# Kernel optimization log

Hardware: AMD Instinct MI355X
Metric: run time of the kernel (lower is better)

Reference implementation:

```python
import jax, jax.numpy as jnp
import numpy as np

B, C, H, W = 4, 512, 128, 128
CI = C // 2   # inter_planes
CQ = C // 8   # q/k dim in CrossAttention


def conv1x1(x, w, b=None):
    # x: [B,Cin,H,W], w: [Cout,Cin]
    y = jnp.einsum('oc,bchw->bohw', w, x)
    if b is not None:
        y = y + b[None, :, None, None]
    return y


def setup_inputs() -> dict:
    key = jax.random.key(0)
    ks = jax.random.split(key, 13)
    s = 0.05
    return {
        'x': jax.random.normal(ks[0], (B, C, H, W), jnp.float32),
        # SCCA gating params (1x1 convs, no bias except conv_up)
        'w_q_right': jax.random.normal(ks[1], (1, C), jnp.float32) * s,
        'w_v_right': jax.random.normal(ks[2], (CI, C), jnp.float32) * s,
        'w_up': jax.random.normal(ks[3], (C, CI), jnp.float32) * s,
        'b_up': jnp.zeros((C,), jnp.float32),
        'w_q_left': jax.random.normal(ks[4], (CI, C), jnp.float32) * s,
        'w_v_left': jax.random.normal(ks[5], (CI, C), jnp.float32) * s,
        # CrossAttention params (1x1 convs with bias)
        'wq': jax.random.normal(ks[6], (CQ, C), jnp.float32) * s,
        'bq': jnp.zeros((CQ,), jnp.float32),
        'wk': jax.random.normal(ks[7], (CQ, C), jnp.float32) * s,
        'bk': jnp.zeros((CQ,), jnp.float32),
        'wv': jax.random.normal(ks[8], (C, C), jnp.float32) * s,
        'bv': jnp.zeros((C,), jnp.float32),
        'gamma': jnp.asarray(0.5, jnp.float32),
    }


def cross_attention(x, wq, bq, wk, bk, wv, bv, gamma):
    # criss-cross attention: each pixel attends to its row and column
    b, c, h, w = x.shape
    q = conv1x1(x, wq, bq)   # [B,CQ,H,W]
    k = conv1x1(x, wk, bk)   # [B,CQ,H,W]
    v = conv1x1(x, wv, bv)   # [B,C,H,W]
    # column (H) affinities with -inf on the self diagonal (as in INF())
    diag = jnp.where(jnp.eye(h, dtype=bool), -jnp.inf, 0.0).astype(x.dtype)
    e_h = jnp.einsum('bchw,bcgw->bhwg', q, k) + diag[None, :, None, :]  # [B,H,W,H]
    e_w = jnp.einsum('bchw,bchv->bhwv', q, k)                            # [B,H,W,W]
    att = jax.nn.softmax(jnp.concatenate([e_h, e_w], axis=-1), axis=-1)  # [B,H,W,H+W]
    a_h, a_w = att[..., :h], att[..., h:]
    out_h = jnp.einsum('bcgw,bhwg->bchw', v, a_h)
    out_w = jnp.einsum('bchv,bhwv->bchw', v, a_w)
    return gamma * (out_h + out_w) + x


def spatial_weighted(x, w_q_right, w_v_right, w_up, b_up):
    b, c, h, w = x.shape
    input_x = conv1x1(x, w_v_right).reshape(b, CI, h * w)       # [B,CI,HW]
    mask = jax.nn.softmax(conv1x1(x, w_q_right).reshape(b, h * w), axis=-1)  # [B,HW]
    ctx = jnp.einsum('bcn,bn->bc', input_x, mask)               # [B,CI]
    ctx = jnp.einsum('oc,bc->bo', w_up, ctx) + b_up             # [B,C]
    mask_ch = jax.nn.sigmoid(ctx)[:, :, None, None]
    return x * mask_ch


def channel_weighted(x, w_q_left, w_v_left):
    b, c, h, w = x.shape
    g_x = conv1x1(x, w_q_left)                                  # [B,CI,H,W]
    avg = g_x.mean(axis=(2, 3))                                 # [B,CI]
    theta = conv1x1(x, w_v_left).reshape(b, CI, h * w)          # [B,CI,HW]
    ctx = jax.nn.softmax(jnp.einsum('bc,bcn->bn', avg, theta), axis=-1)
    mask_sp = jax.nn.sigmoid(ctx).reshape(b, 1, h, w)
    return x * mask_sp


def reference(x, w_q_right, w_v_right, w_up, b_up, w_q_left, w_v_left,
              wq, bq, wk, bk, wv, bv, gamma):
    cc = spatial_weighted(x, w_q_right, w_v_right, w_up, b_up)
    cc = cross_attention(cc, wq, bq, wk, bk, wv, bv, gamma)
    cs = channel_weighted(x, w_q_left, w_v_left)
    cs = cross_attention(cs, wq, bq, wk, bk, wv, bv, gamma)
    out = cs + cc
    out = cross_attention(out, wq, bq, wk, bk, wv, bv, gamma)
    return out
```

## Files before the change

### kernel.cpp

```cpp
#include <hip/hip_runtime.h>
#include <hip/hip_bf16.h>
#include <math.h>

typedef __hip_bfloat16 bf16;
typedef __attribute__((ext_vector_type(8))) short s16x8;
typedef __attribute__((ext_vector_type(4))) float f32x4;

constexpr int Bn  = 4;
constexpr int Cn  = 512;
constexpr int Hn  = 128;
constexpr int Wn  = 128;
constexpr int Nn  = Hn * Wn;
constexpr int CQn = 64;
constexpr int CIn = 256;

__device__ __forceinline__ float bf2f(bf16 v){ return __bfloat162float(v); }
__device__ __forceinline__ bf16  f2bf(float v){ return __float2bfloat16(v); }

__device__ __forceinline__ void gload_lds16(const void* g, void* l){
  __builtin_amdgcn_global_load_lds(
      (const __attribute__((address_space(1))) unsigned int*)g,
      (__attribute__((address_space(3))) unsigned int*)l,
      16, 0, 0);
}


__global__ __launch_bounds__(256) void k_dotc(const float* __restrict__ x,
                                              const float* __restrict__ w,
                                              int wstride,
                                              float* __restrict__ out){
  int t = blockIdx.x * 256 + threadIdx.x;
  int b = t >> 14;
  const float* wp = w + (size_t)b * wstride;
  const float* xp = x + (size_t)b * Cn * Nn + (t & (Nn - 1));
  float acc = 0.f;
  #pragma unroll 8
  for (int c = 0; c < Cn; ++c) acc += wp[c] * xp[(size_t)c * Nn];
  out[t] = acc;
}

__global__ __launch_bounds__(256) void k_rowmean(const float* __restrict__ x,
                                                 float* __restrict__ out,
                                                 float scale){
  int bc = blockIdx.x;
  const float* xp = x + (size_t)bc * Nn;
  float acc = 0.f;
  for (int n = threadIdx.x; n < Nn; n += 256) acc += xp[n];
  for (int o = 32; o > 0; o >>= 1) acc += __shfl_down(acc, o);
  __shared__ float red[4];
  if ((threadIdx.x & 63) == 0) red[threadIdx.x >> 6] = acc;
  __syncthreads();
  if (threadIdx.x == 0) out[bc] = (red[0] + red[1] + red[2] + red[3]) * scale;
}

__global__ __launch_bounds__(256) void k_rowdot(const float* __restrict__ W,
                                                const float* __restrict__ vec,
                                                float* __restrict__ out){
  __shared__ float vs[Cn];
  int b = blockIdx.x, t = threadIdx.x;
  for (int j = t; j < Cn; j += 256) vs[j] = vec[b * Cn + j];
  __syncthreads();
  const float4* wp = (const float4*)(W + (size_t)t * Cn);
  float a = 0.f;
  #pragma unroll 4
  for (int j = 0; j < Cn / 4; ++j){
    float4 w4 = wp[j];
    a += w4.x * vs[4*j] + w4.y * vs[4*j+1] + w4.z * vs[4*j+2] + w4.w * vs[4*j+3];
  }
  out[b * CIn + t] = a;
}

__global__ __launch_bounds__(256) void k_coldot(const float* __restrict__ W,
                                                const float* __restrict__ vec,
                                                float* __restrict__ out){
  __shared__ float vs[CIn];
  int b = blockIdx.y, t = threadIdx.x;
  int c = blockIdx.x * 256 + t;
  if (t < CIn) vs[t] = vec[b * CIn + t];
  __syncthreads();
  float a = 0.f;
  #pragma unroll 8
  for (int j = 0; j < CIn; ++j) a += W[(size_t)j * Cn + c] * vs[j];
  out[b * Cn + c] = a;
}

__global__ __launch_bounds__(256) void k_mch2(const float* __restrict__ w_up,
                                              const float* __restrict__ b_up,
                                              const float* __restrict__ ctx,
                                              float* __restrict__ mch){
  __shared__ float cs[CIn];
  int b = blockIdx.y, t = threadIdx.x;
  int o = blockIdx.x * 256 + t;
  if (t < CIn) cs[t] = ctx[b * CIn + t];
  __syncthreads();
  const float4* wp = (const float4*)(w_up + (size_t)o * CIn);
  float a = b_up[o];
  #pragma unroll 4
  for (int j = 0; j < CIn / 4; ++j){
    float4 w4 = wp[j];
    a += w4.x * cs[4*j] + w4.y * cs[4*j+1] + w4.z * cs[4*j+2] + w4.w * cs[4*j+3];
  }
  mch[b * Cn + o] = 1.f / (1.f + expf(-a));
}

__global__ __launch_bounds__(1024) void k_stats(const float* __restrict__ vv,
                                                float* __restrict__ stats){
  int b = blockIdx.x;
  const float* pp = vv + (size_t)b * Nn;
  int t = threadIdx.x;
  float m = -3.4e38f;
  for (int n = t; n < Nn; n += 1024) m = fmaxf(m, pp[n]);
  for (int o = 32; o > 0; o >>= 1) m = fmaxf(m, __shfl_down(m, o));
  __shared__ float red[16];
  int wid = t >> 6, lid = t & 63;
  if (lid == 0) red[wid] = m;
  __syncthreads();
  if (t == 0){
    float q = red[0];
    for (int i = 1; i < 16; i++) q = fmaxf(q, red[i]);
    red[0] = q;
  }
  __syncthreads();
  m = red[0];
  __syncthreads();
  float s = 0.f;
  for (int n = t; n < Nn; n += 1024) s += expf(pp[n] - m);
  for (int o = 32; o > 0; o >>= 1) s += __shfl_down(s, o);
  if (lid == 0) red[wid] = s;
  __syncthreads();
  if (t == 0){
    float q = 0.f;
    for (int i = 0; i < 16; i++) q += red[i];
    stats[b * 2]     = m;
    stats[b * 2 + 1] = q;
  }
}

__global__ __launch_bounds__(256) void k_weighted(const float* __restrict__ x,
                                                  const float* __restrict__ logits,
                                                  const float* __restrict__ stats,
                                                  float* __restrict__ out){
  int bc = blockIdx.x;
  int b = bc >> 9;
  const float* xp = x + (size_t)bc * Nn;
  const float* lp = logits + (size_t)b * Nn;
  float m = stats[b * 2], den = stats[b * 2 + 1];
  float acc = 0.f;
  for (int n = threadIdx.x; n < Nn; n += 256) acc += xp[n] * expf(lp[n] - m);
  for (int o = 32; o > 0; o >>= 1) acc += __shfl_down(acc, o);
  __shared__ float red[4];
  if ((threadIdx.x & 63) == 0) red[threadIdx.x >> 6] = acc;
  __syncthreads();
  if (threadIdx.x == 0) out[bc] = (red[0] + red[1] + red[2] + red[3]) / den;
}

__global__ __launch_bounds__(256) void k_msp(const float* __restrict__ lg,
                                             const float* __restrict__ stats,
                                             float* __restrict__ msp){
  int t = blockIdx.x * 256 + threadIdx.x;
  int b = t >> 14;
  float v = expf(lg[t] - stats[b * 2]) / stats[b * 2 + 1];
  msp[t] = 1.f / (1.f + expf(-v));
}

__global__ __launch_bounds__(256) void k_applyT3(const float* __restrict__ x,
                                                 const float* __restrict__ mch,
                                                 const float* __restrict__ msp,
                                                 bf16* __restrict__ cc_hi,
                                                 bf16* __restrict__ cc_lo,
                                                 bf16* __restrict__ cs_hi,
                                                 bf16* __restrict__ cs_lo){
  __shared__ bf16 tch[32][33], tcl[32][33], tsh[32][33], tsl[32][33];
  int nt = blockIdx.x, ct = blockIdx.y, b = blockIdx.z;
  int n0 = nt * 32, c0 = ct * 32;
  int t = threadIdx.x;
  #pragma unroll
  for (int kk = 0; kk < 4; ++kk){
    int idx = t + kk * 256;
    int cl = idx >> 5, nl = idx & 31;
    float xv = x[((size_t)(b * Cn + c0 + cl)) * Nn + n0 + nl];
    float ccv = xv * mch[b * Cn + c0 + cl];
    float csv = xv * msp[b * Nn + n0 + nl];
    bf16 h1 = f2bf(ccv);
    tch[cl][nl] = h1;
    tcl[cl][nl] = f2bf(ccv - bf2f(h1));
    bf16 h2 = f2bf(csv);
    tsh[cl][nl] = h2;
    tsl[cl][nl] = f2bf(csv - bf2f(h2));
  }
  __syncthreads();
  #pragma unroll
  for (int kk = 0; kk < 4; ++kk){
    int idx = t + kk * 256;
    int nl = idx >> 5, cl = idx & 31;
    size_t o = ((size_t)(b * Nn + n0 + nl)) * Cn + c0 + cl;
    cc_hi[o] = tch[cl][nl];
    cc_lo[o] = tcl[cl][nl];
    cs_hi[o] = tsh[cl][nl];
    cs_lo[o] = tsl[cl][nl];
  }
}


__global__ __launch_bounds__(256) void k_cvt_w(const float* __restrict__ in,
                                               bf16* __restrict__ out, int n){
  int t = blockIdx.x * 256 + threadIdx.x;
  if (t < n) out[t] = f2bf(in[t]);
}

__global__ __launch_bounds__(256) void k_prep_wqk(const float* __restrict__ wq,
                                                  const float* __restrict__ wk,
                                                  const float* __restrict__ bq,
                                                  const float* __restrict__ bk,
                                                  bf16* __restrict__ wqk_hi,
                                                  bf16* __restrict__ wqk_lo,
                                                  float* __restrict__ bqk){
  int t = blockIdx.x * 256 + threadIdx.x;
  int o = t >> 9, c = t & 511;
  float v = (o < 64) ? wq[(size_t)o * Cn + c] : wk[(size_t)(o - 64) * Cn + c];
  bf16 h = f2bf(v);
  wqk_hi[t] = h;
  wqk_lo[t] = f2bf(v - bf2f(h));
  if (t < 128) bqk[t] = (t < 64) ? bq[t] : bk[t - 64];
}

__global__ __launch_bounds__(256) void k_cvt_T(const float* __restrict__ in,
                                               bf16* __restrict__ out_hi,
                                               bf16* __restrict__ out_lo){
  __shared__ bf16 th_[32][33];
  __shared__ bf16 tl_[32][33];
  int nt = blockIdx.x, ct = blockIdx.y, b = blockIdx.z;
  int n0 = nt * 32, c0 = ct * 32;
  int t = threadIdx.x;
  #pragma unroll
  for (int kk = 0; kk < 4; ++kk){
    int idx = t + kk * 256;
    int cl = idx >> 5, nl = idx & 31;
    float v = in[((size_t)(b * Cn + c0 + cl)) * Nn + n0 + nl];
    bf16 h = f2bf(v);
    th_[cl][nl] = h;
    tl_[cl][nl] = f2bf(v - bf2f(h));
  }
  __syncthreads();
  #pragma unroll
  for (int kk = 0; kk < 4; ++kk){
    int idx = t + kk * 256;
    int nl = idx >> 5, cl = idx & 31;
    size_t o = ((size_t)(b * Nn + n0 + nl)) * Cn + c0 + cl;
    out_hi[o] = th_[cl][nl];
    out_lo[o] = tl_[cl][nl];
  }
}


__global__ __launch_bounds__(256) void k_v_mfma(const bf16* __restrict__ xT,
                                                const bf16* __restrict__ wvb,
                                                const float* __restrict__ bv,
                                                bf16* __restrict__ v){
  __shared__ short As[128 * 64];
  __shared__ short Bs[128 * 64];
  __shared__ float bvs[128];
  int lin = blockIdx.x;
  int swz = (lin & 7) * 256 + (lin >> 3);
  int cb = (swz & 3) * 128;
  int nb = ((swz >> 2) & 127) * 128;
  int b  = swz >> 9;
  int t = threadIdx.x, lane = t & 63, wid = t >> 6;
  int wm = wid >> 1, wn = wid & 1;
  int l15 = lane & 15, l4 = lane >> 4;
  if (t < 128) bvs[t] = bv[cb + t];
  f32x4 acc[4][4];
  #pragma unroll
  for (int i = 0; i < 4; i++)
    #pragma unroll
    for (int j = 0; j < 4; j++) acc[i][j] = (f32x4){0.f, 0.f, 0.f, 0.f};

  const bf16* wp = wvb + (size_t)cb * Cn;
  const bf16* xp = xT + ((size_t)b * Nn + nb) * Cn;
  int r8 = lane >> 3;
  int kc = (lane & 7) * 8;
  for (int kt = 0; kt < 8; ++kt){
    int k0 = kt * 64;
    #pragma unroll
    for (int j = 0; j < 4; ++j){
      int inst = wid * 4 + j;
      int row = inst * 8 + r8;
      gload_lds16(wp + (size_t)row * Cn + k0 + kc, (char*)As + inst * 1024);
      gload_lds16(xp + (size_t)row * Cn + k0 + kc, (char*)Bs + inst * 1024);
    }
    __syncthreads();
    #pragma unroll
    for (int kk = 0; kk < 64; kk += 32){
      s16x8 a[4], bb[4];
      #pragma unroll
      for (int mi = 0; mi < 4; mi++)
        a[mi] = *(const s16x8*)&As[(wm * 64 + mi * 16 + l15) * 64 + kk + l4 * 8];
      #pragma unroll
      for (int ni = 0; ni < 4; ni++)
        bb[ni] = *(const s16x8*)&Bs[(wn * 64 + ni * 16 + l15) * 64 + kk + l4 * 8];
      #pragma unroll
      for (int mi = 0; mi < 4; mi++)
        #pragma unroll
        for (int ni = 0; ni < 4; ni++)
          acc[mi][ni] = __builtin_amdgcn_mfma_f32_16x16x32_bf16(a[mi], bb[ni], acc[mi][ni], 0, 0, 0);
    }
    __syncthreads();
  }
  #pragma unroll
  for (int mi = 0; mi < 4; mi++){
    #pragma unroll
    for (int r = 0; r < 4; r++){
      int cl = wm * 64 + mi * 16 + l4 * 4 + r;
      int c  = cb + cl;
      float bias = bvs[cl];
      #pragma unroll
      for (int ni = 0; ni < 4; ni++){
        int n = nb + wn * 64 + ni * 16 + l15;
        v[((size_t)(b * Cn + c)) * Nn + n] = f2bf(acc[mi][ni][r] + bias);
      }
    }
  }
}

__global__ __launch_bounds__(256) void k_qk_mfma(const bf16* __restrict__ xT_hi,
                                                 const bf16* __restrict__ xT_lo,
                                                 const bf16* __restrict__ wqk_hi,
                                                 const bf16* __restrict__ wqk_lo,
                                                 const float* __restrict__ bqk,
                                                 bf16* __restrict__ qhw,
                                                 bf16* __restrict__ khw){
  __shared__ char smem[65536];
  short* Ah = (short*)smem;
  short* Al = Ah + 8192;
  short* Bh = Al + 8192;
  short* Bl = Bh + 8192;
  char*  Os = smem;
  __shared__ float bs[128];
  int h = blockIdx.x, b = blockIdx.y;
  int nb = h * 128;
  int t = threadIdx.x, lane = t & 63, wid = t >> 6;
  int wm = wid >> 1, wn = wid & 1;
  int l15 = lane & 15, l4 = lane >> 4;
  if (t < 128) bs[t] = bqk[t];
  f32x4 acc[4][4];
  #pragma unroll
  for (int i = 0; i < 4; i++)
    #pragma unroll
    for (int j = 0; j < 4; j++) acc[i][j] = (f32x4){0.f, 0.f, 0.f, 0.f};

  const bf16* xh = xT_hi + ((size_t)b * Nn + nb) * Cn;
  const bf16* xl = xT_lo + ((size_t)b * Nn + nb) * Cn;
  int r8 = lane >> 3;
  int kc = (lane & 7) * 8;
  for (int kt = 0; kt < 8; ++kt){
    int k0 = kt * 64;
    #pragma unroll
    for (int j = 0; j < 4; ++j){
      int inst = wid * 4 + j;
      int row = inst * 8 + r8;
      size_t off = (size_t)row * Cn + k0 + kc;
      gload_lds16(wqk_hi + off, (char*)Ah + inst * 1024);
      gload_lds16(wqk_lo + off, (char*)Al + inst * 1024);
      gload_lds16(xh + off,     (char*)Bh + inst * 1024);
      gload_lds16(xl + off,     (char*)Bl + inst * 1024);
    }
    __syncthreads();
    #pragma unroll
    for (int kk = 0; kk < 64; kk += 32){
      s16x8 ah[4], al[4], bh[4], bl[4];
      #pragma unroll
      for (int mi = 0; mi < 4; mi++){
        int idx = (wm * 64 + mi * 16 + l15) * 64 + kk + l4 * 8;
        ah[mi] = *(const s16x8*)&Ah[idx];
        al[mi] = *(const s16x8*)&Al[idx];
      }
      #pragma unroll
      for (int ni = 0; ni < 4; ni++){
        int idx = (wn * 64 + ni * 16 + l15) * 64 + kk + l4 * 8;
        bh[ni] = *(const s16x8*)&Bh[idx];
        bl[ni] = *(const s16x8*)&Bl[idx];
      }
      #pragma unroll
      for (int mi = 0; mi < 4; mi++)
        #pragma unroll
        for (int ni = 0; ni < 4; ni++){
          acc[mi][ni] = __builtin_amdgcn_mfma_f32_16x16x32_bf16(ah[mi], bh[ni], acc[mi][ni], 0, 0, 0);
          acc[mi][ni] = __builtin_amdgcn_mfma_f32_16x16x32_bf16(ah[mi], bl[ni], acc[mi][ni], 0, 0, 0);
          acc[mi][ni] = __builtin_amdgcn_mfma_f32_16x16x32_bf16(al[mi], bh[ni], acc[mi][ni], 0, 0, 0);
        }
    }
    __syncthreads();
  }
  #pragma unroll
  for (int mi = 0; mi < 4; mi++){
    #pragma unroll
    for (int r = 0; r < 4; r++){
      int o = wm * 64 + mi * 16 + l4 * 4 + r;
      float bias = bs[o];
      #pragma unroll
      for (int ni = 0; ni < 4; ni++){
        int n = wn * 64 + ni * 16 + l15;
        bf16 bv = f2bf(acc[mi][ni][r] + bias);
        int byte = (n * 256 + o * 2) ^ ((n & 7) << 4);
        *(unsigned short*)(Os + byte) = *(unsigned short*)&bv;
      }
    }
  }
  __syncthreads();
  #pragma unroll
  for (int i = 0; i < 8; ++i){
    int s = t + i * 256;
    int row = s >> 3, seg = s & 7;
    int w = row & 127, qk = row >> 7;
    int o0 = qk * 64 + seg * 8;
    int byte = (w * 256 + o0 * 2) ^ ((w & 7) << 4);
    s16x8 d = *(const s16x8*)(Os + byte);
    bf16* dst = (qk == 0 ? qhw : khw) + (((size_t)b * Wn + w) * Hn + h) * CQn + seg * 8;
    *(s16x8*)dst = d;
  }
}


__global__ __launch_bounds__(256) void k_att_h(const bf16* __restrict__ qhw,
                                               const bf16* __restrict__ khw,
                                               const bf16* __restrict__ vT,
                                               float* __restrict__ mh,
                                               float* __restrict__ sh,
                                               bf16* __restrict__ ohX){
  __shared__ char smem[65536];
  char* attb = smem;
  char* vbb  = smem + 32768;
  float* redm = (float*)(smem + 32768);
  float* reds = redm + 256;
  int w = blockIdx.x, b = blockIdx.y;
  int t = threadIdx.x, lane = t & 63, wid = t >> 6;
  int wm = wid >> 1, wn = wid & 1;
  int l15 = lane & 15, l4 = lane >> 4;

  const bf16* qp = qhw + ((size_t)(b * Wn + w)) * (Hn * CQn);
  const bf16* kp = khw + ((size_t)(b * Wn + w)) * (Hn * CQn);
  f32x4 acc[4][4];
  #pragma unroll
  for (int i = 0; i < 4; i++)
    #pragma unroll
    for (int j = 0; j < 4; j++) acc[i][j] = (f32x4){0.f, 0.f, 0.f, 0.f};
  #pragma unroll
  for (int kk = 0; kk < 64; kk += 32){
    s16x8 a[4], bb[4];
    #pragma unroll
    for (int mi = 0; mi < 4; mi++)
      a[mi] = *(const s16x8*)(qp + (size_t)(wm * 64 + mi * 16 + l15) * CQn + kk + l4 * 8);
    #pragma unroll
    for (int ni = 0; ni < 4; ni++)
      bb[ni] = *(const s16x8*)(kp + (size_t)(wn * 64 + ni * 16 + l15) * CQn + kk + l4 * 8);
    #pragma unroll
    for (int mi = 0; mi < 4; mi++)
      #pragma unroll
      for (int ni = 0; ni < 4; ni++)
        acc[mi][ni] = __builtin_amdgcn_mfma_f32_16x16x32_bf16(a[mi], bb[ni], acc[mi][ni], 0, 0, 0);
  }
  if (wm == wn){
    #pragma unroll
    for (int mi = 0; mi < 4; mi++)
      #pragma unroll
      for (int r = 0; r < 4; r++)
        if (l15 == l4 * 4 + r) acc[mi][mi][r] = -1e30f;
  }
  float rm[4][4];
  #pragma unroll
  for (int mi = 0; mi < 4; mi++)
    #pragma unroll
    for (int r = 0; r < 4; r++){
      float m = fmaxf(fmaxf(acc[mi][0][r], acc[mi][1][r]),
                      fmaxf(acc[mi][2][r], acc[mi][3][r]));
      m = fmaxf(m, __shfl_xor(m, 1));
      m = fmaxf(m, __shfl_xor(m, 2));
      m = fmaxf(m, __shfl_xor(m, 4));
      m = fmaxf(m, __shfl_xor(m, 8));
      rm[mi][r] = m;
    }
  if (l15 == 0){
    #pragma unroll
    for (int mi = 0; mi < 4; mi++)
      #pragma unroll
      for (int r = 0; r < 4; r++)
        redm[wn * 128 + wm * 64 + mi * 16 + l4 * 4 + r] = rm[mi][r];
  }
  __syncthreads();
  float rs[4][4];
  #pragma unroll
  for (int mi = 0; mi < 4; mi++)
    #pragma unroll
    for (int r = 0; r < 4; r++){
      int h = wm * 64 + mi * 16 + l4 * 4 + r;
      float m = fmaxf(redm[h], redm[128 + h]);
      rm[mi][r] = m;
      float s = 0.f;
      #pragma unroll
      for (int ni = 0; ni < 4; ni++){
        acc[mi][ni][r] = expf(acc[mi][ni][r] - m);
        s += acc[mi][ni][r];
      }
      s += __shfl_xor(s, 1);
      s += __shfl_xor(s, 2);
      s += __shfl_xor(s, 4);
      s += __shfl_xor(s, 8);
      rs[mi][r] = s;
    }
  if (l15 == 0){
    #pragma unroll
    for (int mi = 0; mi < 4; mi++)
      #pragma unroll
      for (int r = 0; r < 4; r++)
        reds[wn * 128 + wm * 64 + mi * 16 + l4 * 4 + r] = rs[mi][r];
  }
  __syncthreads();
  #pragma unroll
  for (int mi = 0; mi < 4; mi++)
    #pragma unroll
    for (int r = 0; r < 4; r++){
      int h = wm * 64 + mi * 16 + l4 * 4 + r;
      if (wn == 0 && l15 == 0){
        mh[(size_t)(b * Wn + w) * Hn + h] = rm[mi][r];
        sh[(size_t)(b * Wn + w) * Hn + h] = reds[h] + reds[128 + h];
      }
      #pragma unroll
      for (int ni = 0; ni < 4; ni++){
        int g = wn * 64 + ni * 16 + l15;
        bf16 bv = f2bf(acc[mi][ni][r]);
        int byte = (h * 256 + g * 2) ^ ((h & 7) << 4);
        *(unsigned short*)(attb + byte) = *(unsigned short*)&bv;
      }
    }
  __syncthreads();
  for (int cb = 0; cb < Cn; cb += 128){
    const bf16* vp = vT + ((size_t)(b * Wn + w) * Cn + cb) * Hn;
    for (int s = t; s < 2048; s += 256){
      int row = s >> 4, seg = s & 15;
      s16x8 d = *(const s16x8*)(vp + (size_t)row * Hn + seg * 8);
      int byte = (row * 256 + seg * 16) ^ ((row & 7) << 4);
      *(s16x8*)(vbb + byte) = d;
    }
    __syncthreads();
    f32x4 acc2[4][4];
    #pragma unroll
    for (int i = 0; i < 4; i++)
      #pragma unroll
      for (int j = 0; j < 4; j++) acc2[i][j] = (f32x4){0.f, 0.f, 0.f, 0.f};
    #pragma unroll
    for (int kk = 0; kk < 128; kk += 32){
      s16x8 a[4], bb[4];
      #pragma unroll
      for (int mi = 0; mi < 4; mi++){
        int row = wm * 64 + mi * 16 + l15;
        int byte = (row * 256 + (kk + l4 * 8) * 2) ^ ((row & 7) << 4);
        a[mi] = *(const s16x8*)(vbb + byte);
      }
      #pragma unroll
      for (int ni = 0; ni < 4; ni++){
        int row = wn * 64 + ni * 16 + l15;
        int byte = (row * 256 + (kk + l4 * 8) * 2) ^ ((row & 7) << 4);
        bb[ni] = *(const s16x8*)(attb + byte);
      }
      #pragma unroll
      for (int mi = 0; mi < 4; mi++)
        #pragma unroll
        for (int ni = 0; ni < 4; ni++)
          acc2[mi][ni] = __builtin_amdgcn_mfma_f32_16x16x32_bf16(a[mi], bb[ni], acc2[mi][ni], 0, 0, 0);
    }
    bf16* op = ohX + ((size_t)(b * Cn + cb)) * Nn + (size_t)w * Hn;
    #pragma unroll
    for (int mi = 0; mi < 4; mi++)
      #pragma unroll
      for (int r = 0; r < 4; r++){
        int cl = wm * 64 + mi * 16 + l4 * 4 + r;
        #pragma unroll
        for (int ni = 0; ni < 4; ni++){
          int h = wn * 64 + ni * 16 + l15;
          op[(size_t)cl * Nn + h] = f2bf(acc2[mi][ni][r]);
        }
      }
    __syncthreads();
  }
}

__global__ __launch_bounds__(256) void k_att_w(const bf16* __restrict__ qhw,
                                               const bf16* __restrict__ khw,
                                               const bf16* __restrict__ v,
                                               float* __restrict__ mw,
                                               float* __restrict__ sw,
                                               bf16* __restrict__ ow){
  __shared__ char smem[65536];
  char* attb = smem;
  char* vbb  = smem + 32768;
  float* redm = (float*)(smem + 32768);
  float* reds = redm + 256;
  int h = blockIdx.x, b = blockIdx.y;
  int t = threadIdx.x, lane = t & 63, wid = t >> 6;
  int wm = wid >> 1, wn = wid & 1;
  int l15 = lane & 15, l4 = lane >> 4;

  const bf16* qp = qhw + (size_t)b * Wn * Hn * CQn + (size_t)h * CQn;
  const bf16* kp = khw + (size_t)b * Wn * Hn * CQn + (size_t)h * CQn;
  f32x4 acc[4][4];
  #pragma unroll
  for (int i = 0; i < 4; i++)
    #pragma unroll
    for (int j = 0; j < 4; j++) acc[i][j] = (f32x4){0.f, 0.f, 0.f, 0.f};
  #pragma unroll
  for (int kk = 0; kk < 64; kk += 32){
    s16x8 a[4], bb[4];
    #pragma unroll
    for (int mi = 0; mi < 4; mi++)
      a[mi] = *(const s16x8*)(qp + (size_t)(wm * 64 + mi * 16 + l15) * (Hn * CQn) + kk + l4 * 8);
    #pragma unroll
    for (int ni = 0; ni < 4; ni++)
      bb[ni] = *(const s16x8*)(kp + (size_t)(wn * 64 + ni * 16 + l15) * (Hn * CQn) + kk + l4 * 8);
    #pragma unroll
    for (int mi = 0; mi < 4; mi++)
      #pragma unroll
      for (int ni = 0; ni < 4; ni++)
        acc[mi][ni] = __builtin_amdgcn_mfma_f32_16x16x32_bf16(a[mi], bb[ni], acc[mi][ni], 0, 0, 0);
  }
  float rm[4][4];
  #pragma unroll
  for (int mi = 0; mi < 4; mi++)
    #pragma unroll
    for (int r = 0; r < 4; r++){
      float m = fmaxf(fmaxf(acc[mi][0][r], acc[mi][1][r]),
                      fmaxf(acc[mi][2][r], acc[mi][3][r]));
      m = fmaxf(m, __shfl_xor(m, 1));
      m = fmaxf(m, __shfl_xor(m, 2));
      m = fmaxf(m, __shfl_xor(m, 4));
      m = fmaxf(m, __shfl_xor(m, 8));
      rm[mi][r] = m;
    }
  if (l15 == 0){
    #pragma unroll
    for (int mi = 0; mi < 4; mi++)
      #pragma unroll
      for (int r = 0; r < 4; r++)
        redm[wn * 128 + wm * 64 + mi * 16 + l4 * 4 + r] = rm[mi][r];
  }
  __syncthreads();
  float rs[4][4];
  #pragma unroll
  for (int mi = 0; mi < 4; mi++)
    #pragma unroll
    for (int r = 0; r < 4; r++){
      int wr = wm * 64 + mi * 16 + l4 * 4 + r;
      float m = fmaxf(redm[wr], redm[128 + wr]);
      rm[mi][r] = m;
      float s = 0.f;
      #pragma unroll
      for (int ni = 0; ni < 4; ni++){
        acc[mi][ni][r] = expf(acc[mi][ni][r] - m);
        s += acc[mi][ni][r];
      }
      s += __shfl_xor(s, 1);
      s += __shfl_xor(s, 2);
      s += __shfl_xor(s, 4);
      s += __shfl_xor(s, 8);
      rs[mi][r] = s;
    }
  if (l15 == 0){
    #pragma unroll
    for (int mi = 0; mi < 4; mi++)
      #pragma unroll
      for (int r = 0; r < 4; r++)
        reds[wn * 128 + wm * 64 + mi * 16 + l4 * 4 + r] = rs[mi][r];
  }
  __syncthreads();
  #pragma unroll
  for (int mi = 0; mi < 4; mi++)
    #pragma unroll
    for (int r = 0; r < 4; r++){
      int wr = wm * 64 + mi * 16 + l4 * 4 + r;
      if (wn == 0 && l15 == 0){
        mw[(size_t)(b * Hn + h) * Wn + wr] = rm[mi][r];
        sw[(size_t)(b * Hn + h) * Wn + wr] = reds[wr] + reds[128 + wr];
      }
      #pragma unroll
      for (int ni = 0; ni < 4; ni++){
        int g = wn * 64 + ni * 16 + l15;
        bf16 bv = f2bf(acc[mi][ni][r]);
        int byte = (wr * 256 + g * 2) ^ ((wr & 7) << 4);
        *(unsigned short*)(attb + byte) = *(unsigned short*)&bv;
      }
    }
  __syncthreads();
  for (int cb = 0; cb < Cn; cb += 128){
    const bf16* vp = v + (size_t)(b * Cn + cb) * Nn + (size_t)h * Wn;
    for (int s = t; s < 2048; s += 256){
      int row = s >> 4, seg = s & 15;
      s16x8 d = *(const s16x8*)(vp + (size_t)row * Nn + seg * 8);
      int byte = (row * 256 + seg * 16) ^ ((row & 7) << 4);
      *(s16x8*)(vbb + byte) = d;
    }
    __syncthreads();
    f32x4 acc2[4][4];
    #pragma unroll
    for (int i = 0; i < 4; i++)
      #pragma unroll
      for (int j = 0; j < 4; j++) acc2[i][j] = (f32x4){0.f, 0.f, 0.f, 0.f};
    #pragma unroll
    for (int kk = 0; kk < 128; kk += 32){
      s16x8 a[4], bb[4];
      #pragma unroll
      for (int mi = 0; mi < 4; mi++){
        int row = wm * 64 + mi * 16 + l15;
        int byte = (row * 256 + (kk + l4 * 8) * 2) ^ ((row & 7) << 4);
        a[mi] = *(const s16x8*)(vbb + byte);
      }
      #pragma unroll
      for (int ni = 0; ni < 4; ni++){
        int row = wn * 64 + ni * 16 + l15;
        int byte = (row * 256 + (kk + l4 * 8) * 2) ^ ((row & 7) << 4);
        bb[ni] = *(const s16x8*)(attb + byte);
      }
      #pragma unroll
      for (int mi = 0; mi < 4; mi++)
        #pragma unroll
        for (int ni = 0; ni < 4; ni++)
          acc2[mi][ni] = __builtin_amdgcn_mfma_f32_16x16x32_bf16(a[mi], bb[ni], acc2[mi][ni], 0, 0, 0);
    }
    bf16* op = ow + (size_t)(b * Cn + cb) * Nn + (size_t)h * Wn;
    #pragma unroll
    for (int mi = 0; mi < 4; mi++)
      #pragma unroll
      for (int r = 0; r < 4; r++){
        int cl = wm * 64 + mi * 16 + l4 * 4 + r;
        #pragma unroll
        for (int ni = 0; ni < 4; ni++){
          int wr = wn * 64 + ni * 16 + l15;
          op[(size_t)cl * Nn + wr] = f2bf(acc2[mi][ni][r]);
        }
      }
    __syncthreads();
  }
}

__global__ __launch_bounds__(256) void k_alpha(const float* __restrict__ mh,
                                               const float* __restrict__ sh,
                                               const float* __restrict__ mw,
                                               const float* __restrict__ sw,
                                               float* __restrict__ ahT,
                                               float* __restrict__ aw){
  int t = blockIdx.x * 256 + threadIdx.x;
  int b = t >> 14;
  int hw = t & (Nn - 1);
  int h = hw >> 7, w = hw & 127;
  size_t ih = (size_t)(b * Wn + w) * Hn + h;
  size_t iw = t;
  float mhv = mh[ih], mwv = mw[iw];
  float M = fmaxf(mhv, mwv);
  float eh_ = expf(mhv - M), ew_ = expf(mwv - M);
  float inv = 1.f / (sh[ih] * eh_ + sw[iw] * ew_);
  ahT[t] = eh_ * inv;
  aw[t]  = ew_ * inv;
}


__global__ __launch_bounds__(256) void k_trans(const bf16* __restrict__ in,
                                               bf16* __restrict__ out,
                                               int CH){
  __shared__ bf16 tile[32][33];
  int tl = blockIdx.x, c = blockIdx.y, b = blockIdx.z;
  int th = tl >> 2, tw = tl & 3;
  int h0 = th * 32, w0 = tw * 32;
  int t = threadIdx.x;
  const bf16* ip = in + ((size_t)(b * CH + c)) * Nn;
  #pragma unroll
  for (int kk = 0; kk < 4; ++kk){
    int idx = t + kk * 256;
    int hl = idx >> 5, wl = idx & 31;
    tile[hl][wl] = ip[(h0 + hl) * Wn + w0 + wl];
  }
  __syncthreads();
  #pragma unroll
  for (int kk = 0; kk < 4; ++kk){
    int idx = t + kk * 256;
    int wl = idx >> 5, hl = idx & 31;
    out[((size_t)(b * Wn + w0 + wl) * CH + c) * Hn + h0 + hl] = tile[hl][wl];
  }
}

__global__ __launch_bounds__(256) void k_fuse2(const float* __restrict__ in,
                                               const float* __restrict__ maskc,
                                               const float* __restrict__ maskn,
                                               const bf16* __restrict__ ohX,
                                               const bf16* __restrict__ ow,
                                               const float* __restrict__ ahT,
                                               const float* __restrict__ aw,
                                               const float* __restrict__ addend,
                                               const float* __restrict__ gamma,
                                               float* __restrict__ out){
  __shared__ unsigned short tileT[64][138];
  int c = blockIdx.x, half = blockIdx.y, b = blockIdx.z;
  int t = threadIdx.x;
  float g = gamma[0];
  float mc = maskc ? maskc[b * Cn + c] : 1.f;
  int h0 = half * 64;
  const bf16* ohp = ohX + ((size_t)(b * Cn + c)) * Nn;
  #pragma unroll
  for (int i = 0; i < 4; ++i){
    int s = t + i * 256;
    int w = s >> 3, seg = s & 7;
    s16x8 d = *(const s16x8*)(ohp + (size_t)w * Hn + h0 + seg * 8);
    #pragma unroll
    for (int j = 0; j < 8; ++j)
      tileT[seg * 8 + j][w] = (unsigned short)d[j];
  }
  __syncthreads();
  size_t base = ((size_t)(b * Cn + c)) * Nn;
  #pragma unroll
  for (int i = 0; i < 8; ++i){
    int o = t + i * 256;
    int hl = o >> 5, w4 = (o & 31) * 4;
    int h = h0 + hl;
    size_t idx = base + (size_t)h * Wn + w4;
    size_t aidx = (size_t)b * Nn + (size_t)h * Wn + w4;
    ushort4 owv = *(const ushort4*)((const unsigned short*)ow + idx);
    float4 ah4 = *(const float4*)(ahT + aidx);
    float4 aw4 = *(const float4*)(aw + aidx);
    float4 inv = in ? *(const float4*)(in + idx) : (float4){0.f,0.f,0.f,0.f};
    float4 mn4 = maskn ? *(const float4*)(maskn + aidx) : (float4){1.f,1.f,1.f,1.f};
    float r[4];
    #pragma unroll
    for (int j = 0; j < 4; ++j){
      unsigned short uh = tileT[hl][w4 + j];
      unsigned short uo = ((const unsigned short*)&owv)[j];
      float ohv = bf2f(*(bf16*)&uh);
      float owf = bf2f(*(bf16*)&uo);
      float xv  = ((const float*)&inv)[j];
      float mnv = ((const float*)&mn4)[j];
      float iv;
      if (!in)                 iv = 0.f;
      else if (maskc && maskn) iv = xv * (mc + mnv);
      else                     iv = xv * mc * mnv;
      float ahv = ((const float*)&ah4)[j];
      float awv = ((const float*)&aw4)[j];
      r[j] = g * (ahv * ohv + awv * owf) + iv;
    }
    if (addend){
      float4 av = *(const float4*)(addend + idx);
      r[0] += av.x; r[1] += av.y; r[2] += av.z; r[3] += av.w;
    }
    float4 o4 = { r[0], r[1], r[2], r[3] };
    *(float4*)(out + idx) = o4;
  }
}


static void run_ca(const float* resid, const float* maskc, const float* maskn,
                   const bf16* wqk_hi, const bf16* wqk_lo,
                   const float* bqk, const bf16* wvb, const float* bv,
                   const float* gamma, const float* addend, float* out,
                   bf16* qhw, bf16* khw, bf16* v, bf16* vT,
                   float* mh, float* sh, float* mw, float* sw, float* ahT, float* aw,
                   const bf16* xT_hi, const bf16* xT_lo, bf16* tmp, hipStream_t stream){
  bf16* ohX = tmp;
  bf16* ow  = tmp + (size_t)Bn * Cn * Nn;
  k_qk_mfma<<<dim3(Nn / 128, Bn), 256, 0, stream>>>(xT_hi, xT_lo, wqk_hi, wqk_lo, bqk,
                                                    qhw, khw);
  k_v_mfma<<<2048, 256, 0, stream>>>(xT_hi, wvb, bv, v);
  k_trans<<<dim3(16, Cn, Bn), 256, 0, stream>>>(v, vT, Cn);
  k_att_h<<<dim3(Wn, Bn), 256, 0, stream>>>(qhw, khw, vT, mh, sh, ohX);
  k_att_w<<<dim3(Hn, Bn), 256, 0, stream>>>(qhw, khw, v, mw, sw, ow);
  k_alpha<<<Bn * Nn / 256, 256, 0, stream>>>(mh, sh, mw, sw, ahT, aw);
  k_fuse2<<<dim3(Cn, 2, Bn), 256, 0, stream>>>(resid, maskc, maskn, ohX, ow, ahT, aw,
                                               addend, gamma, out);
}

extern "C" void kernel_launch(void* const* d_in, const int* in_sizes, int n_in,
                              void* d_out, int out_size, void* d_ws, size_t ws_size,
                              hipStream_t stream){
  (void)in_sizes; (void)n_in; (void)out_size; (void)ws_size;
  const float* x         = (const float*)d_in[0];
  const float* w_q_right = (const float*)d_in[1];
  const float* w_v_right = (const float*)d_in[2];
  const float* w_up      = (const float*)d_in[3];
  const float* b_up      = (const float*)d_in[4];
  const float* w_q_left  = (const float*)d_in[5];
  const float* w_v_left  = (const float*)d_in[6];
  const float* wq        = (const float*)d_in[7];
  const float* bq        = (const float*)d_in[8];
  const float* wk        = (const float*)d_in[9];
  const float* bk        = (const float*)d_in[10];
  const float* wv        = (const float*)d_in[11];
  const float* bv        = (const float*)d_in[12];
  const float* gamma     = (const float*)d_in[13];

  const size_t SZ_MAP = (size_t)Bn * Cn * Nn;
  char* p = (char*)d_ws;
  float* buf0   = (float*)p; p += SZ_MAP * 4;
  float* buf1   = (float*)p; p += SZ_MAP * 4;
  bf16*  vbuf   = (bf16*)p;  p += SZ_MAP * 2;
  bf16*  vT     = (bf16*)p;  p += SZ_MAP * 2;
  bf16*  qhw    = (bf16*)p;  p += (size_t)Bn * CQn * Nn * 2;
  bf16*  khw    = (bf16*)p;  p += (size_t)Bn * CQn * Nn * 2;
  float* ebuf   = (float*)p; p += (size_t)SZ_MAP * 2;
  float* logits = (float*)p; p += (size_t)Bn * Nn * 4;
  float* ctxlog = (float*)p; p += (size_t)Bn * Nn * 4;
  float* msp    = (float*)p; p += (size_t)Bn * Nn * 4;
  float* xbar   = (float*)p; p += Bn * Cn * 4;
  float* wgt    = (float*)p; p += Bn * Cn * 4;
  float* u      = (float*)p; p += Bn * Cn * 4;
  float* mch    = (float*)p; p += Bn * Cn * 4;
  float* avg    = (float*)p; p += Bn * CIn * 4;
  float* ctx    = (float*)p; p += Bn * CIn * 4;
  float* stats_sp = (float*)p; p += 64;
  float* stats_ch = (float*)p; p += 64;
  bf16*  wvb    = (bf16*)p;  p += (size_t)Cn * Cn * 2;
  bf16*  wqk_hi = (bf16*)p;  p += (size_t)128 * Cn * 2;
  bf16*  wqk_lo = (bf16*)p;  p += (size_t)128 * Cn * 2;
  float* bqk    = (float*)p; p += 128 * 4;
  float* mh     = (float*)p; p += (size_t)Bn * Nn * 4;
  float* sh     = (float*)p; p += (size_t)Bn * Nn * 4;
  float* mw     = (float*)p; p += (size_t)Bn * Nn * 4;
  float* sw     = (float*)p; p += (size_t)Bn * Nn * 4;
  float* ahT    = (float*)p; p += (size_t)Bn * Nn * 4;
  float* aw     = (float*)p; p += (size_t)Bn * Nn * 4;

  bf16*  cc_hi  = (bf16*)ebuf;
  bf16*  cc_lo  = (bf16*)d_out;
  bf16*  cs_hi  = (bf16*)buf1;
  bf16*  cs_lo  = (bf16*)buf1 + SZ_MAP;
  bf16*  xT_hi3 = (bf16*)ebuf;
  bf16*  xT_lo3 = (bf16*)d_out;

  k_cvt_w<<<(Cn * Cn + 255) / 256, 256, 0, stream>>>(wv, wvb, Cn * Cn);
  k_prep_wqk<<<(128 * Cn) / 256, 256, 0, stream>>>(wq, wk, bq, bk, wqk_hi, wqk_lo, bqk);

  k_dotc<<<Bn * Nn / 256, 256, 0, stream>>>(x, w_q_right, 0, logits);
  k_rowmean<<<Bn * Cn, 256, 0, stream>>>(x, xbar, 1.f / Nn);
  k_rowdot<<<Bn, 256, 0, stream>>>(w_q_left, xbar, avg);
  k_coldot<<<dim3(Cn / 256, Bn), 256, 0, stream>>>(w_v_left, avg, u);
  k_stats<<<Bn, 1024, 0, stream>>>(logits, stats_sp);
  k_weighted<<<Bn * Cn, 256, 0, stream>>>(x, logits, stats_sp, wgt);
  k_rowdot<<<Bn, 256, 0, stream>>>(w_v_right, wgt, ctx);
  k_mch2<<<dim3(Cn / 256, Bn), 256, 0, stream>>>(w_up, b_up, ctx, mch);
  k_dotc<<<Bn * Nn / 256, 256, 0, stream>>>(x, u, Cn, ctxlog);
  k_stats<<<Bn, 1024, 0, stream>>>(ctxlog, stats_ch);
  k_msp<<<Bn * Nn / 256, 256, 0, stream>>>(ctxlog, stats_ch, msp);

  k_applyT3<<<dim3(Nn / 32, Cn / 32, Bn), 256, 0, stream>>>(x, mch, msp,
                                                            cc_hi, cc_lo, cs_hi, cs_lo);

  run_ca(nullptr, nullptr, nullptr, wqk_hi, wqk_lo, bqk, wvb, bv, gamma, nullptr, buf0,
         qhw, khw, vbuf, vT, mh, sh, mw, sw, ahT, aw,
         cc_hi, cc_lo, (bf16*)d_out, stream);
  run_ca(x, mch, msp, wqk_hi, wqk_lo, bqk, wvb, bv, gamma, buf0, buf0,
         qhw, khw, vbuf, vT, mh, sh, mw, sw, ahT, aw,
         cs_hi, cs_lo, (bf16*)d_out, stream);
  k_cvt_T<<<dim3(Nn / 32, Cn / 32, Bn), 256, 0, stream>>>(buf0, xT_hi3, xT_lo3);
  run_ca(buf0, nullptr, nullptr, wqk_hi, wqk_lo, bqk, wvb, bv, gamma, nullptr,
         (float*)d_out,
         qhw, khw, vbuf, vT, mh, sh, mw, sw, ahT, aw,
         xT_hi3, xT_lo3, (bf16*)buf1, stream);
}
```

Measured before the change: 1.357 ms.

## Fuse first two criss-cross attention epilogues into one combine kernel

The epilogues of the cc and cs attention passes are merged into a new k_fuse3 kernel. It reads both attention outputs and both sets of alpha weights and writes the summed result once. This removes one fp32 write and two re-reads of the intermediate buffer, plus a kernel launch. In exchange it needs extra alpha buffers and a new buffer-aliasing plan across d_out, buf0 and buf1, which could be wrong if any of those buffers overlap the cs inputs.

```diff
diff --git a/kernel.cpp b/kernel.cpp
--- a/kernel.cpp
+++ b/kernel.cpp
@@ -786,20 +786,16 @@
 }
 
 __global__ __launch_bounds__(256) void k_fuse2(const float* __restrict__ in,
-                                               const float* __restrict__ maskc,
-                                               const float* __restrict__ maskn,
                                                const bf16* __restrict__ ohX,
                                                const bf16* __restrict__ ow,
                                                const float* __restrict__ ahT,
                                                const float* __restrict__ aw,
-                                               const float* __restrict__ addend,
                                                const float* __restrict__ gamma,
                                                float* __restrict__ out){
   __shared__ unsigned short tileT[64][138];
   int c = blockIdx.x, half = blockIdx.y, b = blockIdx.z;
   int t = threadIdx.x;
   float g = gamma[0];
-  float mc = maskc ? maskc[b * Cn + c] : 1.f;
   int h0 = half * 64;
   const bf16* ohp = ohX + ((size_t)(b * Cn + c)) * Nn;
   #pragma unroll
@@ -824,7 +820,6 @@
     float4 ah4 = *(const float4*)(ahT + aidx);
     float4 aw4 = *(const float4*)(aw + aidx);
     float4 inv = in ? *(const float4*)(in + idx) : (float4){0.f,0.f,0.f,0.f};
-    float4 mn4 = maskn ? *(const float4*)(maskn + aidx) : (float4){1.f,1.f,1.f,1.f};
     float r[4];
     #pragma unroll
     for (int j = 0; j < 4; ++j){
@@ -832,33 +827,92 @@
       unsigned short uo = ((const unsigned short*)&owv)[j];
       float ohv = bf2f(*(bf16*)&uh);
       float owf = bf2f(*(bf16*)&uo);
-      float xv  = ((const float*)&inv)[j];
-      float mnv = ((const float*)&mn4)[j];
-      float iv;
-      if (!in)                 iv = 0.f;
-      else if (maskc && maskn) iv = xv * (mc + mnv);
-      else                     iv = xv * mc * mnv;
       float ahv = ((const float*)&ah4)[j];
       float awv = ((const float*)&aw4)[j];
-      r[j] = g * (ahv * ohv + awv * owf) + iv;
-    }
-    if (addend){
-      float4 av = *(const float4*)(addend + idx);
-      r[0] += av.x; r[1] += av.y; r[2] += av.z; r[3] += av.w;
+      r[j] = g * (ahv * ohv + awv * owf) + ((const float*)&inv)[j];
     }
     float4 o4 = { r[0], r[1], r[2], r[3] };
     *(float4*)(out + idx) = o4;
   }
 }
 
-
-static void run_ca(const float* resid, const float* maskc, const float* maskn,
-                   const bf16* wqk_hi, const bf16* wqk_lo,
-                   const float* bqk, const bf16* wvb, const float* bv,
-                   const float* gamma, const float* addend, float* out,
-                   bf16* qhw, bf16* khw, bf16* v, bf16* vT,
-                   float* mh, float* sh, float* mw, float* sw, float* ahT, float* aw,
-                   const bf16* xT_hi, const bf16* xT_lo, bf16* tmp, hipStream_t stream){
+__global__ __launch_bounds__(256) void k_fuse3(const float* __restrict__ x,
+                                               const float* __restrict__ mch,
+                                               const float* __restrict__ msp,
+                                               const bf16* __restrict__ oh1,
+                                               const bf16* __restrict__ ow1,
+                                               const float* __restrict__ a1h,
+                                               const float* __restrict__ a1w,
+                                               const bf16* __restrict__ oh2,
+                                               const bf16* __restrict__ ow2,
+                                               const float* __restrict__ a2h,
+                                               const float* __restrict__ a2w,
+                                               const float* __restrict__ gamma,
+                                               float* __restrict__ out){
+  __shared__ unsigned short t1[64][138];
+  __shared__ unsigned short t2[64][138];
+  int c = blockIdx.x, half = blockIdx.y, b = blockIdx.z;
+  int t = threadIdx.x;
+  float g = gamma[0];
+  float mc = mch[b * Cn + c];
+  int h0 = half * 64;
+  const bf16* p1 = oh1 + ((size_t)(b * Cn + c)) * Nn;
+  const bf16* p2 = oh2 + ((size_t)(b * Cn + c)) * Nn;
+  #pragma unroll
+  for (int i = 0; i < 4; ++i){
+    int s = t + i * 256;
+    int w = s >> 3, seg = s & 7;
+    s16x8 d1 = *(const s16x8*)(p1 + (size_t)w * Hn + h0 + seg * 8);
+    s16x8 d2 = *(const s16x8*)(p2 + (size_t)w * Hn + h0 + seg * 8);
+    #pragma unroll
+    for (int j = 0; j < 8; ++j){
+      t1[seg * 8 + j][w] = (unsigned short)d1[j];
+      t2[seg * 8 + j][w] = (unsigned short)d2[j];
+    }
+  }
+  __syncthreads();
+  size_t base = ((size_t)(b * Cn + c)) * Nn;
+  #pragma unroll
+  for (int i = 0; i < 8; ++i){
+    int o = t + i * 256;
+    int hl = o >> 5, w4 = (o & 31) * 4;
+    int h = h0 + hl;
+    size_t idx = base + (size_t)h * Wn + w4;
+    size_t aidx = (size_t)b * Nn + (size_t)h * Wn + w4;
+    ushort4 o1v = *(const ushort4*)((const unsigned short*)ow1 + idx);
+    ushort4 o2v = *(const ushort4*)((const unsigned short*)ow2 + idx);
+    float4 a1h4 = *(const float4*)(a1h + aidx);
+    float4 a1w4 = *(const float4*)(a1w + aidx);
+    float4 a2h4 = *(const float4*)(a2h + aidx);
+    float4 a2w4 = *(const float4*)(a2w + aidx);
+    float4 xv4  = *(const float4*)(x + idx);
+    float4 mn4  = *(const float4*)(msp + aidx);
+    float r[4];
+    #pragma unroll
+    for (int j = 0; j < 4; ++j){
+      unsigned short u1 = t1[hl][w4 + j];
+      unsigned short u2 = t2[hl][w4 + j];
+      unsigned short w1 = ((const unsigned short*)&o1v)[j];
+      unsigned short w2 = ((const unsigned short*)&o2v)[j];
+      float oh1v = bf2f(*(bf16*)&u1), ow1v = bf2f(*(bf16*)&w1);
+      float oh2v = bf2f(*(bf16*)&u2), ow2v = bf2f(*(bf16*)&w2);
+      float term1 = g * (((const float*)&a1h4)[j] * oh1v + ((const float*)&a1w4)[j] * ow1v);
+      float term2 = g * (((const float*)&a2h4)[j] * oh2v + ((const float*)&a2w4)[j] * ow2v);
+      float resid = ((const float*)&xv4)[j] * (mc + ((const float*)&mn4)[j]);
+      r[j] = term2 + resid + term1;
+    }
+    float4 o4 = { r[0], r[1], r[2], r[3] };
+    *(float4*)(out + idx) = o4;
+  }
+}
+
+
+static void run_att(const bf16* xT_hi, const bf16* xT_lo,
+                    const bf16* wqk_hi, const bf16* wqk_lo, const float* bqk,
+                    const bf16* wvb, const float* bv,
+                    bf16* qhw, bf16* khw, bf16* v, bf16* vT,
+                    float* mh, float* sh, float* mw, float* sw,
+                    float* ahT, float* aw, bf16* tmp, hipStream_t stream){
   bf16* ohX = tmp;
   bf16* ow  = tmp + (size_t)Bn * Cn * Nn;
   k_qk_mfma<<<dim3(Nn / 128, Bn), 256, 0, stream>>>(xT_hi, xT_lo, wqk_hi, wqk_lo, bqk,
@@ -868,8 +922,6 @@
   k_att_h<<<dim3(Wn, Bn), 256, 0, stream>>>(qhw, khw, vT, mh, sh, ohX);
   k_att_w<<<dim3(Hn, Bn), 256, 0, stream>>>(qhw, khw, v, mw, sw, ow);
   k_alpha<<<Bn * Nn / 256, 256, 0, stream>>>(mh, sh, mw, sw, ahT, aw);
-  k_fuse2<<<dim3(Cn, 2, Bn), 256, 0, stream>>>(resid, maskc, maskn, ohX, ow, ahT, aw,
-                                               addend, gamma, out);
 }
 
 extern "C" void kernel_launch(void* const* d_in, const int* in_sizes, int n_in,
@@ -919,8 +971,10 @@
   float* sh     = (float*)p; p += (size_t)Bn * Nn * 4;
   float* mw     = (float*)p; p += (size_t)Bn * Nn * 4;
   float* sw     = (float*)p; p += (size_t)Bn * Nn * 4;
-  float* ahT    = (float*)p; p += (size_t)Bn * Nn * 4;
-  float* aw     = (float*)p; p += (size_t)Bn * Nn * 4;
+  float* ah1    = (float*)p; p += (size_t)Bn * Nn * 4;
+  float* aw1    = (float*)p; p += (size_t)Bn * Nn * 4;
+  float* ah2    = (float*)p; p += (size_t)Bn * Nn * 4;
+  float* aw2    = (float*)p; p += (size_t)Bn * Nn * 4;
 
   bf16*  cc_hi  = (bf16*)ebuf;
   bf16*  cc_lo  = (bf16*)d_out;
@@ -947,15 +1001,20 @@
   k_applyT3<<<dim3(Nn / 32, Cn / 32, Bn), 256, 0, stream>>>(x, mch, msp,
                                                             cc_hi, cc_lo, cs_hi, cs_lo);
 
-  run_ca(nullptr, nullptr, nullptr, wqk_hi, wqk_lo, bqk, wvb, bv, gamma, nullptr, buf0,
-         qhw, khw, vbuf, vT, mh, sh, mw, sw, ahT, aw,
-         cc_hi, cc_lo, (bf16*)d_out, stream);
-  run_ca(x, mch, msp, wqk_hi, wqk_lo, bqk, wvb, bv, gamma, buf0, buf0,
-         qhw, khw, vbuf, vT, mh, sh, mw, sw, ahT, aw,
-         cs_hi, cs_lo, (bf16*)d_out, stream);
-  k_cvt_T<<<dim3(Nn / 32, Cn / 32, Bn), 256, 0, stream>>>(buf0, xT_hi3, xT_lo3);
-  run_ca(buf0, nullptr, nullptr, wqk_hi, wqk_lo, bqk, wvb, bv, gamma, nullptr,
-         (float*)d_out,
-         qhw, khw, vbuf, vT, mh, sh, mw, sw, ahT, aw,
-         xT_hi3, xT_lo3, (bf16*)buf1, stream);
-}
+  run_att(cc_hi, cc_lo, wqk_hi, wqk_lo, bqk, wvb, bv,
+          qhw, khw, vbuf, vT, mh, sh, mw, sw, ah1, aw1, (bf16*)d_out, stream);
+  run_att(cs_hi, cs_lo, wqk_hi, wqk_lo, bqk, wvb, bv,
+          qhw, khw, vbuf, vT, mh, sh, mw, sw, ah2, aw2, (bf16*)buf0, stream);
+  k_fuse3<<<dim3(Cn, 2, Bn), 256, 0, stream>>>(x, mch, msp,
+                                               (const bf16*)d_out,
+                                               (const bf16*)d_out + SZ_MAP, ah1, aw1,
+                                               (const bf16*)buf0,
+                                               (const bf16*)buf0 + SZ_MAP, ah2, aw2,
+                                               gamma, buf1);
+  k_cvt_T<<<dim3(Nn / 32, Cn / 32, Bn), 256, 0, stream>>>(buf1, xT_hi3, xT_lo3);
+  run_att(xT_hi3, xT_lo3, wqk_hi, wqk_lo, bqk, wvb, bv,
+          qhw, khw, vbuf, vT, mh, sh, mw, sw, ah1, aw1, (bf16*)buf0, stream);
+  k_fuse2<<<dim3(Cn, 2, Bn), 256, 0, stream>>>(buf1, (const bf16*)buf0,
+                                               (const bf16*)buf0 + SZ_MAP, ah1, aw1,
+                                               gamma, (float*)d_out);
+}
```

Result: faster. 1.274 ms, median of 2 (-6.2%).
